# Optimization experiments

Measured on AMD Instinct MI355X. Metric: run time of the kernel, lower is better.

The kernel has to match this reference:

```python
import jax, jax.numpy as jnp
import numpy as np
from jax import lax

NPOINT, RADIUS, NSAMPLE, EPS = 2048, 0.1, 32, 1e-5


def setup_inputs() -> dict:
    key = jax.random.key(0)
    ks = jax.random.split(key, 8)
    B, N, D, CIN, COUT, DEPTH = 4, 8192, 29, 32, 64, 2
    return {
        "xyz": jax.random.uniform(ks[0], (B, 3, N), jnp.float32),
        "points": jax.random.normal(ks[1], (B, D, N), jnp.float32),
        "proj_w": jax.random.normal(ks[2], (COUT, CIN), jnp.float32) * 0.05,
        "proj_g": jnp.ones((COUT,), jnp.float32),
        "proj_b": jnp.zeros((COUT,), jnp.float32),
        "w1": jax.random.normal(ks[3], (DEPTH, COUT, COUT), jnp.float32) * 0.05,
        "g1": jnp.ones((DEPTH, COUT), jnp.float32),
        "b1": jnp.zeros((DEPTH, COUT), jnp.float32),
        "w2": jax.random.normal(ks[4], (DEPTH, COUT, COUT), jnp.float32) * 0.05,
        "g2": jnp.ones((DEPTH, COUT), jnp.float32),
        "b2": jnp.zeros((DEPTH, COUT), jnp.float32),
    }


def fps(xyz, npoint):
    # xyz: [B,N,3] -> idx [B,npoint]; deterministic start at index 0
    B, N, _ = xyz.shape
    def body(carry, _):
        dist, far = carry  # [B,N], [B]
        centroid = jnp.take_along_axis(xyz, far[:, None, None], axis=1)  # [B,1,3]
        d = jnp.sum((xyz - centroid) ** 2, -1)
        dist = jnp.minimum(dist, d)
        return (dist, jnp.argmax(dist, -1).astype(jnp.int32)), far
    init = (jnp.full((B, N), 1e10, xyz.dtype), jnp.zeros((B,), jnp.int32))
    _, idx = lax.scan(body, init, None, length=npoint)
    return jnp.transpose(idx)  # [B,npoint]


def ball_query(radius, nsample, xyz, new_xyz):
    # matches torch query_ball_point: invalid -> N, sort, take first nsample, backfill
    N = xyz.shape[1]
    sqr = (jnp.sum(new_xyz ** 2, -1)[:, :, None]
           + jnp.sum(xyz ** 2, -1)[:, None, :]
           - 2.0 * jnp.einsum("bsc,bnc->bsn", new_xyz, xyz))  # [B,S,N]
    cand = jnp.where(sqr <= radius * radius, jnp.arange(N, dtype=jnp.int32), jnp.int32(N))
    neg, _ = lax.top_k(-cand, nsample)
    idx = -neg  # nsample smallest indices, ascending
    first = idx[:, :, :1]
    return jnp.where(idx == N, first, idx)  # [B,S,K]


def gather_nb(p, idx):
    # p [B,N,C], idx [B,S,K] -> [B,S,K,C]
    return jax.vmap(lambda pb, ib: pb[ib])(p, idx)


def _conv(x, w):
    # 1x1 conv: w [O,C], x [B,C,K,S]
    return jnp.einsum("oc,bcks->boks", w, x)


def _bn(x, g, b):
    # training-mode BatchNorm2d over (B,K,S) per channel
    m = jnp.mean(x, (0, 2, 3), keepdims=True)
    v = jnp.var(x, (0, 2, 3), keepdims=True)
    return g[None, :, None, None] * (x - m) * lax.rsqrt(v + EPS) + b[None, :, None, None]


def reference(xyz, points, proj_w, proj_g, proj_b, w1, g1, b1, w2, g2, b2):
    xyz_t = jnp.transpose(xyz, (0, 2, 1))      # [B,N,3]
    pts_t = jnp.transpose(points, (0, 2, 1))   # [B,N,D]
    fidx = fps(xyz_t, NPOINT)                  # [B,S]
    new_xyz = jnp.take_along_axis(xyz_t, fidx[:, :, None], axis=1)  # [B,S,3]
    idx = ball_query(RADIUS, NSAMPLE, xyz_t, new_xyz)               # [B,S,K]
    grouped_xyz = gather_nb(xyz_t, idx) - new_xyz[:, :, None, :]    # [B,S,K,3]
    grouped_pts = gather_nb(pts_t, idx)                             # [B,S,K,D]
    new_points = jnp.concatenate([grouped_xyz, grouped_pts], -1)    # [B,S,K,3+D]
    x = jnp.transpose(new_points, (0, 3, 2, 1))                     # [B,C,K,S]
    x = jax.nn.relu(_bn(_conv(x, proj_w), proj_g, proj_b))
    for d in range(w1.shape[0]):
        idn = x
        x = jax.nn.relu(_bn(_conv(x, w1[d]), g1[d], b1[d]))
        x = _bn(_conv(x, w2[d]), g2[d], b2[d])
        x = jax.nn.relu(x + idn)
    feat = jnp.max(x, axis=2)                  # [B,Cout,S]
    return jnp.transpose(new_xyz, (0, 2, 1)), feat
```

## Files before the change

kernel.cpp:

```cpp
#include <hip/hip_runtime.h>
#include <cstdint>
#include <cstddef>

#define NPTS    8192
#define NPT     2048
#define KNB     32
#define NB      4
#define DPTS    29
#define CINP    32
#define CO      64
#define KS      (KNB*NPT)
#define TELEM   ((size_t)NB*CO*KS)
#define MCNT    262144.0f
#define BNEPS   1e-5f
#define FTHR    1024
#define FWAVES  (FTHR/64)
#define FPT     8

#define FPS_STEP(J)                                                      \
    {                                                                    \
        float dx = __fsub_rn(px##J, cx);                                 \
        float dy = __fsub_rn(py##J, cy);                                 \
        float dz = __fsub_rn(pz##J, cz);                                 \
        float dd = __fadd_rn(__fadd_rn(__fmul_rn(dx, dx),                \
                                       __fmul_rn(dy, dy)),               \
                             __fmul_rn(dz, dz));                         \
        float nd = fminf(d##J, dd);                                      \
        d##J = nd;                                                       \
        bool gt = nd > tb;                                               \
        tb = gt ? nd : tb;                                               \
        jj = gt ? J : jj;                                                \
    }

#define DPP64_MAX(k, ctrl, rmask)                                               \
    {                                                                           \
        unsigned _lo = (unsigned)(k);                                           \
        unsigned _hi = (unsigned)((k) >> 32);                                   \
        _lo = (unsigned)__builtin_amdgcn_update_dpp(0, (int)_lo, ctrl, rmask, 0xf, true); \
        _hi = (unsigned)__builtin_amdgcn_update_dpp(0, (int)_hi, ctrl, rmask, 0xf, true); \
        unsigned long long _k2 = ((unsigned long long)_hi << 32) | _lo;         \
        k = (_k2 > k) ? _k2 : k;                                                \
    }

static __device__ __forceinline__ unsigned long long umax64(unsigned long long a,
                                                            unsigned long long b) {
    return a > b ? a : b;
}

__global__ __launch_bounds__(FTHR, 1)
void fps_kernel(const float* __restrict__ xyz,
                float* __restrict__ out0) {
    const int b = blockIdx.x;
    const int t = threadIdx.x;
    const int lane = t & 63;
    const int wid  = t >> 6;
    const float* xb = xyz + (size_t)b * 3 * NPTS;
    const int base = t * FPT;

    extern __shared__ float smem[];
    float* sx = smem;
    float* sy = sx + NPTS;
    float* sz = sy + NPTS;
    float* so = sz + NPTS;
    unsigned long long* skey = (unsigned long long*)(so + 3 * NPT);

    float px0,px1,px2,px3,px4,px5,px6,px7;
    float py0,py1,py2,py3,py4,py5,py6,py7;
    float pz0,pz1,pz2,pz3,pz4,pz5,pz6,pz7;
    float d0,d1,d2,d3,d4,d5,d6,d7;
    {
        const float4* x4 = (const float4*)(xb + base);
        const float4* y4 = (const float4*)(xb + NPTS + base);
        const float4* z4 = (const float4*)(xb + 2 * NPTS + base);
        float4* lx4 = (float4*)(sx + base);
        float4* ly4 = (float4*)(sy + base);
        float4* lz4 = (float4*)(sz + base);
        float4 v;
        v = x4[0]; lx4[0] = v; px0 =v.x; px1 =v.y; px2 =v.z; px3 =v.w;
        v = x4[1]; lx4[1] = v; px4 =v.x; px5 =v.y; px6 =v.z; px7 =v.w;
        v = y4[0]; ly4[0] = v; py0 =v.x; py1 =v.y; py2 =v.z; py3 =v.w;
        v = y4[1]; ly4[1] = v; py4 =v.x; py5 =v.y; py6 =v.z; py7 =v.w;
        v = z4[0]; lz4[0] = v; pz0 =v.x; pz1 =v.y; pz2 =v.z; pz3 =v.w;
        v = z4[1]; lz4[1] = v; pz4 =v.x; pz5 =v.y; pz6 =v.z; pz7 =v.w;
        d0=d1=d2=d3=d4=d5=d6=d7 = 1e10f;
    }

    float cx = xb[0], cy = xb[NPTS], cz = xb[2 * NPTS];
    if (t == 0) { so[0] = cx; so[NPT] = cy; so[2 * NPT] = cz; }

    for (int i = 1; i < NPT; ++i) {
        float tb = -1.0f;
        int   jj = 0;
        FPS_STEP(0) FPS_STEP(1) FPS_STEP(2) FPS_STEP(3)
        FPS_STEP(4) FPS_STEP(5) FPS_STEP(6) FPS_STEP(7)

        unsigned long long k =
            (((unsigned long long)__float_as_uint(tb)) << 32) |
            (unsigned int)(~(unsigned int)(base + jj));
        DPP64_MAX(k, 0x111, 0xf)
        DPP64_MAX(k, 0x112, 0xf)
        DPP64_MAX(k, 0x114, 0xf)
        DPP64_MAX(k, 0x118, 0xf)
        DPP64_MAX(k, 0x142, 0xa)
        DPP64_MAX(k, 0x143, 0xc)

        const int par = i & 1;
        if (lane == 63) skey[par * FWAVES + wid] = k;
        __syncthreads();

        const ulonglong2* sk2 = (const ulonglong2*)(skey + par * FWAVES);
        ulonglong2 k0 = sk2[0], k1 = sk2[1], k2 = sk2[2], k3 = sk2[3];
        ulonglong2 k4 = sk2[4], k5 = sk2[5], k6 = sk2[6], k7 = sk2[7];
        unsigned long long m0 = umax64(k0.x, k0.y);
        unsigned long long m1 = umax64(k1.x, k1.y);
        unsigned long long m2 = umax64(k2.x, k2.y);
        unsigned long long m3 = umax64(k3.x, k3.y);
        unsigned long long m4 = umax64(k4.x, k4.y);
        unsigned long long m5 = umax64(k5.x, k5.y);
        unsigned long long m6 = umax64(k6.x, k6.y);
        unsigned long long m7 = umax64(k7.x, k7.y);
        unsigned long long kbest = umax64(umax64(umax64(m0, m1), umax64(m2, m3)),
                                          umax64(umax64(m4, m5), umax64(m6, m7)));
        const int widx = (int)(~(unsigned int)kbest);

        cx = sx[widx]; cy = sy[widx]; cz = sz[widx];
        if (t == 0) { so[i] = cx; so[NPT + i] = cy; so[2 * NPT + i] = cz; }
    }

    __syncthreads();
    float* ob = out0 + (size_t)b * 3 * NPT;
    for (int r = t; r < 3 * NPT; r += FTHR) ob[r] = so[r];
}

__global__ __launch_bounds__(256) void ballq_kernel(const float* __restrict__ xyz,
                                                    const float* __restrict__ out0,
                                                    int* __restrict__ idx) {
    const int gw   = (blockIdx.x * 256 + threadIdx.x) >> 6;
    const int lane = threadIdx.x & 63;
    const int b  = gw >> 11;
    const int si = gw & 2047;
    const float* xb = xyz + (size_t)b * 3 * NPTS;

    const float cx = out0[b * 3 * NPT + si];
    const float cy = out0[b * 3 * NPT + NPT + si];
    const float cz = out0[b * 3 * NPT + 2*NPT + si];
    const float csum = __fadd_rn(__fadd_rn(__fmul_rn(cx, cx), __fmul_rn(cy, cy)),
                                 __fmul_rn(cz, cz));
    const float R2 = (float)(0.1 * 0.1);

    __shared__ int buf[4][KNB];
    int* mybuf = buf[threadIdx.x >> 6];

    int cnt = 0;
    for (int n0 = 0; n0 < NPTS && cnt < KNB; n0 += 64) {
        const int i = n0 + lane;
        float pxv = xb[i], pyv = xb[NPTS + i], pzv = xb[2 * NPTS + i];
        float ps = __fadd_rn(__fadd_rn(__fmul_rn(pxv, pxv), __fmul_rn(pyv, pyv)),
                             __fmul_rn(pzv, pzv));
        float dot = __fmaf_rn(pzv, cz, __fmaf_rn(pyv, cy, __fmul_rn(pxv, cx)));
        float sqr = __fsub_rn(__fadd_rn(csum, ps), __fadd_rn(dot, dot));
        bool hit = (sqr <= R2);
        unsigned long long m = __ballot(hit);
        int pos = cnt + __popcll(m & ((1ull << lane) - 1ull));
        if (hit && pos < KNB) mybuf[pos] = i;
        cnt += __popcll(m);
    }
    __syncthreads();
    int c = cnt < KNB ? cnt : KNB;
    int first = (cnt > 0) ? mybuf[0] : 0;
    if (lane < KNB) {
        int v = (lane < c) ? mybuf[lane] : first;
        idx[((size_t)gw << 5) + lane] = v;
    }
}

__global__ __launch_bounds__(256) void proj_kernel(const float* __restrict__ xyz,
                                                   const float* __restrict__ points,
                                                   const float* __restrict__ out0,
                                                   const int* __restrict__ idx,
                                                   const float* __restrict__ W,
                                                   float* __restrict__ out,
                                                   float* __restrict__ stats) {
    const int p = blockIdx.x * 256 + threadIdx.x;
    const int b = p >> 16;
    const int q = p & 65535;
    const int k = q >> 11;
    const int s = q & 2047;
    const int tid = threadIdx.x;

    __shared__ float ssum[CO], ssq[CO];
    if (tid < CO) { ssum[tid] = 0.f; ssq[tid] = 0.f; }
    __syncthreads();

    const int j = idx[((size_t)(b * NPT + s) << 5) + k];
    const float* xb = xyz + (size_t)b * 3 * NPTS;
    float a[CINP];
    a[0] = xb[j]            - out0[b * 3 * NPT + s];
    a[1] = xb[NPTS + j]     - out0[b * 3 * NPT + NPT + s];
    a[2] = xb[2*NPTS + j]   - out0[b * 3 * NPT + 2*NPT + s];
    const float* pb = points + (size_t)b * DPTS * NPTS;
#pragma unroll
    for (int c = 0; c < DPTS; ++c) a[3 + c] = pb[c * NPTS + j];

    const size_t obase = (size_t)b * CO * KS + q;
    for (int o = 0; o < CO; ++o) {
        float acc = 0.f;
#pragma unroll
        for (int c = 0; c < CINP; ++c) acc = __fmaf_rn(W[o * CINP + c], a[c], acc);
        out[obase + (size_t)o * KS] = acc;
        float s1 = acc, s2 = acc * acc;
#pragma unroll
        for (int off = 32; off > 0; off >>= 1) {
            s1 += __shfl_xor(s1, off, 64);
            s2 += __shfl_xor(s2, off, 64);
        }
        if ((tid & 63) == 0) { atomicAdd(&ssum[o], s1); atomicAdd(&ssq[o], s2); }
    }
    __syncthreads();
    if (tid < CO) {
        atomicAdd(&stats[tid], ssum[tid]);
        atomicAdd(&stats[CO + tid], ssq[tid]);
    }
}

template <bool HAS_IDN, bool WRITE_ACT>
__global__ __launch_bounds__(256) void conv_bn_kernel(const float* in,
                                                      const float* idn,
                                                      const float* __restrict__ stats_in,
                                                      const float* __restrict__ gamma,
                                                      const float* __restrict__ beta,
                                                      const float* __restrict__ W,
                                                      float* act_out,
                                                      float* out,
                                                      float* __restrict__ stats_out) {
    const int p = blockIdx.x * 256 + threadIdx.x;
    const int b = p >> 16;
    const int q = p & 65535;
    const int tid = threadIdx.x;

    __shared__ float ssc[CO], ssh[CO], ssum[CO], ssq[CO];
    if (tid < CO) {
        const float Minv = 1.0f / MCNT;
        float m = stats_in[tid] * Minv;
        float v = stats_in[CO + tid] * Minv - m * m;
        float scl = gamma[tid] * rsqrtf(v + BNEPS);
        ssc[tid] = scl;
        ssh[tid] = beta[tid] - m * scl;
        ssum[tid] = 0.f; ssq[tid] = 0.f;
    }
    __syncthreads();

    const size_t base = (size_t)b * CO * KS + q;
    float a[CO];
#pragma unroll
    for (int c = 0; c < CO; ++c) {
        float v = __fmaf_rn(ssc[c], in[base + (size_t)c * KS], ssh[c]);
        if (HAS_IDN) v += idn[base + (size_t)c * KS];
        v = fmaxf(v, 0.0f);
        a[c] = v;
        if (WRITE_ACT) act_out[base + (size_t)c * KS] = v;
    }
    for (int o = 0; o < CO; ++o) {
        float acc = 0.f;
#pragma unroll
        for (int c = 0; c < CO; ++c) acc = __fmaf_rn(W[o * CO + c], a[c], acc);
        out[base + (size_t)o * KS] = acc;
        float s1 = acc, s2 = acc * acc;
#pragma unroll
        for (int off = 32; off > 0; off >>= 1) {
            s1 += __shfl_xor(s1, off, 64);
            s2 += __shfl_xor(s2, off, 64);
        }
        if ((tid & 63) == 0) { atomicAdd(&ssum[o], s1); atomicAdd(&ssq[o], s2); }
    }
    __syncthreads();
    if (tid < CO) {
        atomicAdd(&stats_out[tid], ssum[tid]);
        atomicAdd(&stats_out[CO + tid], ssq[tid]);
    }
}

__global__ __launch_bounds__(256) void final_kernel(const float* __restrict__ y2,
                                                    const float* __restrict__ idn,
                                                    const float* __restrict__ stats,
                                                    const float* __restrict__ gamma,
                                                    const float* __restrict__ beta,
                                                    float* __restrict__ feat) {
    const int p = blockIdx.x * 256 + threadIdx.x;
    const int s = p & 2047;
    const int o = (p >> 11) & 63;
    const int b = p >> 17;
    const float Minv = 1.0f / MCNT;
    float m = stats[o] * Minv;
    float v = stats[CO + o] * Minv - m * m;
    float scl = gamma[o] * rsqrtf(v + BNEPS);
    float sh  = beta[o] - m * scl;
    const size_t base = (size_t)b * CO * KS + (size_t)o * KS + s;
    float mx = -1e30f;
#pragma unroll
    for (int k = 0; k < KNB; ++k) {
        float val = __fmaf_rn(scl, y2[base + (size_t)k * NPT], sh) + idn[base + (size_t)k * NPT];
        val = fmaxf(val, 0.0f);
        mx = fmaxf(mx, val);
    }
    feat[p] = mx;
}

__global__ void zero_kernel(float* p, int n) {
    int i = blockIdx.x * blockDim.x + threadIdx.x;
    if (i < n) p[i] = 0.f;
}

extern "C" void kernel_launch(void* const* d_in, const int* in_sizes, int n_in,
                              void* d_out, int out_size, void* d_ws, size_t ws_size,
                              hipStream_t stream) {
    (void)in_sizes; (void)n_in; (void)out_size; (void)ws_size;
    const float* xyz    = (const float*)d_in[0];
    const float* points = (const float*)d_in[1];
    const float* proj_w = (const float*)d_in[2];
    const float* proj_g = (const float*)d_in[3];
    const float* proj_b = (const float*)d_in[4];
    const float* w1     = (const float*)d_in[5];
    const float* g1     = (const float*)d_in[6];
    const float* b1     = (const float*)d_in[7];
    const float* w2     = (const float*)d_in[8];
    const float* g2     = (const float*)d_in[9];
    const float* b2     = (const float*)d_in[10];

    float* out0 = (float*)d_out;
    float* feat = (float*)d_out + NB * 3 * NPT;

    float* stats = (float*)d_ws;
    int*   idx   = (int*)((float*)d_ws + 1024);
    float* A     = (float*)(idx + NB * NPT * KNB);
    float* B     = A + TELEM;

    const size_t fps_lds = (size_t)(3 * NPTS + 3 * NPT) * sizeof(float)
                         + 2 * FWAVES * sizeof(unsigned long long);

    hipLaunchKernelGGL(zero_kernel, dim3(3), dim3(256), 0, stream, stats, 5 * 2 * CO);
    hipLaunchKernelGGL(fps_kernel, dim3(NB), dim3(FTHR), fps_lds, stream, xyz, out0);
    hipLaunchKernelGGL(ballq_kernel, dim3(2048), dim3(256), 0, stream, xyz, out0, idx);
    hipLaunchKernelGGL(proj_kernel, dim3(1024), dim3(256), 0, stream,
                       xyz, points, out0, idx, proj_w, A, stats);
    hipLaunchKernelGGL((conv_bn_kernel<false, true>), dim3(1024), dim3(256), 0, stream,
                       A, (const float*)nullptr, stats, proj_g, proj_b, w1,
                       B, A, stats + 128);
    hipLaunchKernelGGL((conv_bn_kernel<false, false>), dim3(1024), dim3(256), 0, stream,
                       A, (const float*)nullptr, stats + 128, g1, b1, w2,
                       (float*)nullptr, A, stats + 256);
    hipLaunchKernelGGL((conv_bn_kernel<true, true>), dim3(1024), dim3(256), 0, stream,
                       A, B, stats + 256, g2, b2, w1 + CO * CO,
                       B, A, stats + 384);
    hipLaunchKernelGGL((conv_bn_kernel<false, false>), dim3(1024), dim3(256), 0, stream,
                       A, (const float*)nullptr, stats + 384, g1 + CO, b1 + CO, w2 + CO * CO,
                       (float*)nullptr, A, stats + 512);
    hipLaunchKernelGGL(final_kernel, dim3(2048), dim3(256), 0, stream,
                       A, B, stats + 512, g2 + CO, b2 + CO, feat);
}
```

Baseline: 2.838 ms.

## Use packed FP32 math in FPS and reduce the argmax in one wave

```diff
diff --git a/kernel.cpp b/kernel.cpp
--- a/kernel.cpp
+++ b/kernel.cpp
@@ -17,19 +17,28 @@
 #define FWAVES  (FTHR/64)
 #define FPT     8
 
-#define FPS_STEP(J)                                                      \
+typedef float v2f __attribute__((ext_vector_type(2)));
+
+static __device__ __forceinline__ v2f pk_add(v2f a, v2f b) {
+    v2f d;
+    asm("v_pk_add_f32 %0, %1, %2" : "=v"(d) : "v"(a), "v"(b));
+    return d;
+}
+static __device__ __forceinline__ v2f pk_mul(v2f a, v2f b) {
+    v2f d;
+    asm("v_pk_mul_f32 %0, %1, %2" : "=v"(d) : "v"(a), "v"(b));
+    return d;
+}
+
+#define FPS_PAIR(J)                                                      \
     {                                                                    \
-        float dx = __fsub_rn(px##J, cx);                                 \
-        float dy = __fsub_rn(py##J, cy);                                 \
-        float dz = __fsub_rn(pz##J, cz);                                 \
-        float dd = __fadd_rn(__fadd_rn(__fmul_rn(dx, dx),                \
-                                       __fmul_rn(dy, dy)),               \
-                             __fmul_rn(dz, dz));                         \
-        float nd = fminf(d##J, dd);                                      \
-        d##J = nd;                                                       \
-        bool gt = nd > tb;                                               \
-        tb = gt ? nd : tb;                                               \
-        jj = gt ? J : jj;                                                \
+        v2f dx = pk_add(px##J, cvx);                                     \
+        v2f dy = pk_add(py##J, cvy);                                     \
+        v2f dz = pk_add(pz##J, cvz);                                     \
+        v2f dd = pk_add(pk_add(pk_mul(dx, dx), pk_mul(dy, dy)),          \
+                        pk_mul(dz, dz));                                 \
+        d##J.x = fminf(d##J.x, dd.x);                                    \
+        d##J.y = fminf(d##J.y, dd.y);                                    \
     }
 
 #define DPP64_MAX(k, ctrl, rmask)                                               \
@@ -63,11 +72,10 @@
     float* sz = sy + NPTS;
     float* so = sz + NPTS;
     unsigned long long* skey = (unsigned long long*)(so + 3 * NPT);
-
-    float px0,px1,px2,px3,px4,px5,px6,px7;
-    float py0,py1,py2,py3,py4,py5,py6,py7;
-    float pz0,pz1,pz2,pz3,pz4,pz5,pz6,pz7;
-    float d0,d1,d2,d3,d4,d5,d6,d7;
+    float* swin = (float*)(skey + FWAVES);
+
+    v2f px01, px23, px45, px67, py01, py23, py45, py67, pz01, pz23, pz45, pz67;
+    v2f d01, d23, d45, d67;
     {
         const float4* x4 = (const float4*)(xb + base);
         const float4* y4 = (const float4*)(xb + NPTS + base);
@@ -76,23 +84,35 @@
         float4* ly4 = (float4*)(sy + base);
         float4* lz4 = (float4*)(sz + base);
         float4 v;
-        v = x4[0]; lx4[0] = v; px0 =v.x; px1 =v.y; px2 =v.z; px3 =v.w;
-        v = x4[1]; lx4[1] = v; px4 =v.x; px5 =v.y; px6 =v.z; px7 =v.w;
-        v = y4[0]; ly4[0] = v; py0 =v.x; py1 =v.y; py2 =v.z; py3 =v.w;
-        v = y4[1]; ly4[1] = v; py4 =v.x; py5 =v.y; py6 =v.z; py7 =v.w;
-        v = z4[0]; lz4[0] = v; pz0 =v.x; pz1 =v.y; pz2 =v.z; pz3 =v.w;
-        v = z4[1]; lz4[1] = v; pz4 =v.x; pz5 =v.y; pz6 =v.z; pz7 =v.w;
-        d0=d1=d2=d3=d4=d5=d6=d7 = 1e10f;
+        v = x4[0]; lx4[0] = v; px01 = (v2f){v.x, v.y}; px23 = (v2f){v.z, v.w};
+        v = x4[1]; lx4[1] = v; px45 = (v2f){v.x, v.y}; px67 = (v2f){v.z, v.w};
+        v = y4[0]; ly4[0] = v; py01 = (v2f){v.x, v.y}; py23 = (v2f){v.z, v.w};
+        v = y4[1]; ly4[1] = v; py45 = (v2f){v.x, v.y}; py67 = (v2f){v.z, v.w};
+        v = z4[0]; lz4[0] = v; pz01 = (v2f){v.x, v.y}; pz23 = (v2f){v.z, v.w};
+        v = z4[1]; lz4[1] = v; pz45 = (v2f){v.x, v.y}; pz67 = (v2f){v.z, v.w};
+        d01 = d23 = d45 = d67 = (v2f){1e10f, 1e10f};
     }
 
     float cx = xb[0], cy = xb[NPTS], cz = xb[2 * NPTS];
     if (t == 0) { so[0] = cx; so[NPT] = cy; so[2 * NPT] = cz; }
 
     for (int i = 1; i < NPT; ++i) {
-        float tb = -1.0f;
-        int   jj = 0;
-        FPS_STEP(0) FPS_STEP(1) FPS_STEP(2) FPS_STEP(3)
-        FPS_STEP(4) FPS_STEP(5) FPS_STEP(6) FPS_STEP(7)
+        const float ncx = -cx, ncy = -cy, ncz = -cz;
+        const v2f cvx = (v2f){ncx, ncx};
+        const v2f cvy = (v2f){ncy, ncy};
+        const v2f cvz = (v2f){ncz, ncz};
+        FPS_PAIR(01) FPS_PAIR(23) FPS_PAIR(45) FPS_PAIR(67)
+
+        float tb = fmaxf(fmaxf(fmaxf(d01.x, d01.y), fmaxf(d23.x, d23.y)),
+                         fmaxf(fmaxf(d45.x, d45.y), fmaxf(d67.x, d67.y)));
+        int jj = 7;
+        if (d67.x == tb) jj = 6;
+        if (d45.y == tb) jj = 5;
+        if (d45.x == tb) jj = 4;
+        if (d23.y == tb) jj = 3;
+        if (d23.x == tb) jj = 2;
+        if (d01.y == tb) jj = 1;
+        if (d01.x == tb) jj = 0;
 
         unsigned long long k =
             (((unsigned long long)__float_as_uint(tb)) << 32) |
@@ -103,28 +123,32 @@
         DPP64_MAX(k, 0x118, 0xf)
         DPP64_MAX(k, 0x142, 0xa)
         DPP64_MAX(k, 0x143, 0xc)
-
-        const int par = i & 1;
-        if (lane == 63) skey[par * FWAVES + wid] = k;
+        if (lane == 63) skey[wid] = k;
         __syncthreads();
 
-        const ulonglong2* sk2 = (const ulonglong2*)(skey + par * FWAVES);
-        ulonglong2 k0 = sk2[0], k1 = sk2[1], k2 = sk2[2], k3 = sk2[3];
-        ulonglong2 k4 = sk2[4], k5 = sk2[5], k6 = sk2[6], k7 = sk2[7];
-        unsigned long long m0 = umax64(k0.x, k0.y);
-        unsigned long long m1 = umax64(k1.x, k1.y);
-        unsigned long long m2 = umax64(k2.x, k2.y);
-        unsigned long long m3 = umax64(k3.x, k3.y);
-        unsigned long long m4 = umax64(k4.x, k4.y);
-        unsigned long long m5 = umax64(k5.x, k5.y);
-        unsigned long long m6 = umax64(k6.x, k6.y);
-        unsigned long long m7 = umax64(k7.x, k7.y);
-        unsigned long long kbest = umax64(umax64(umax64(m0, m1), umax64(m2, m3)),
-                                          umax64(umax64(m4, m5), umax64(m6, m7)));
-        const int widx = (int)(~(unsigned int)kbest);
-
-        cx = sx[widx]; cy = sy[widx]; cz = sz[widx];
-        if (t == 0) { so[i] = cx; so[NPT + i] = cy; so[2 * NPT + i] = cz; }
+        if (wid == 0) {
+            const ulonglong2* sk2 = (const ulonglong2*)skey;
+            ulonglong2 k0 = sk2[0], k1 = sk2[1], k2 = sk2[2], k3 = sk2[3];
+            ulonglong2 k4 = sk2[4], k5 = sk2[5], k6 = sk2[6], k7 = sk2[7];
+            unsigned long long m0 = umax64(k0.x, k0.y);
+            unsigned long long m1 = umax64(k1.x, k1.y);
+            unsigned long long m2 = umax64(k2.x, k2.y);
+            unsigned long long m3 = umax64(k3.x, k3.y);
+            unsigned long long m4 = umax64(k4.x, k4.y);
+            unsigned long long m5 = umax64(k5.x, k5.y);
+            unsigned long long m6 = umax64(k6.x, k6.y);
+            unsigned long long m7 = umax64(k7.x, k7.y);
+            unsigned long long kbest = umax64(umax64(umax64(m0, m1), umax64(m2, m3)),
+                                              umax64(umax64(m4, m5), umax64(m6, m7)));
+            const int widx = (int)(~(unsigned int)kbest);
+            float wx = sx[widx], wy = sy[widx], wz = sz[widx];
+            if (t == 0) {
+                swin[0] = wx; swin[1] = wy; swin[2] = wz;
+                so[i] = wx; so[NPT + i] = wy; so[2 * NPT + i] = wz;
+            }
+        }
+        __syncthreads();
+        cx = swin[0]; cy = swin[1]; cz = swin[2];
     }
 
     __syncthreads();
@@ -336,7 +360,8 @@
     float* B     = A + TELEM;
 
     const size_t fps_lds = (size_t)(3 * NPTS + 3 * NPT) * sizeof(float)
-                         + 2 * FWAVES * sizeof(unsigned long long);
+                         + FWAVES * sizeof(unsigned long long)
+                         + 4 * sizeof(float);
 
     hipLaunchKernelGGL(zero_kernel, dim3(3), dim3(256), 0, stream, stats, 5 * 2 * CO);
     hipLaunchKernelGGL(fps_kernel, dim3(NB), dim3(FTHR), fps_lds, stream, xyz, out0);
```

Result: slower. 3.153 ms (+11.1%).
